# Performance work log

Measured on AMD Instinct MI355X. Metric: run time of the kernel, lower is better.

The kernel has to match this reference:

```python
import jax, jax.numpy as jnp
import numpy as np

E = 1024      # embed_dim
H = 16        # num_heads
D = E // H    # head_dim
SCALING = float(D * 1.0) ** (-0.5)


def setup_inputs() -> dict:
    key = jax.random.key(0)
    ks = jax.random.split(key, 10)
    B, L, S = 4, 2048, 2048
    query = jax.random.normal(ks[0], (B, L, E), dtype=jnp.float32)
    k_in = jax.random.normal(ks[1], (B, S, E), dtype=jnp.float32)
    v_in = jax.random.normal(ks[2], (B, S, E), dtype=jnp.float32)
    attn_bias = jax.random.normal(ks[3], (L, S), dtype=jnp.float32)
    attn_mask = jax.random.normal(ks[4], (L, S), dtype=jnp.float32)
    # in_proj: Linear(E, 3E)  (xavier-uniform-ish scale), out_proj: Linear(E, E)
    lim_in = np.sqrt(6.0 / (E + 3 * E))
    Wqkv = jax.random.uniform(ks[5], (3 * E, E), minval=-lim_in, maxval=lim_in, dtype=jnp.float32)
    bqkv = jnp.zeros((3 * E,), dtype=jnp.float32)
    lim_out = np.sqrt(1.0 / E)
    Wo = jax.random.uniform(ks[6], (E, E), minval=-lim_out, maxval=lim_out, dtype=jnp.float32)
    bo = jnp.zeros((E,), dtype=jnp.float32)
    return {"query": query, "key": k_in, "value": v_in,
            "attn_bias": attn_bias, "attn_mask": attn_mask,
            "Wqkv": Wqkv, "bqkv": bqkv, "Wo": Wo, "bo": bo}


def reference(query, key, value, attn_bias, attn_mask, Wqkv, bqkv, Wo, bo):
    B, L, _ = query.shape
    S = key.shape[1]
    # fused in_proj split into q/k/v slices (q from query, k from key, v from value)
    q = query @ Wqkv[:E].T + bqkv[:E]
    k = key @ Wqkv[E:2 * E].T + bqkv[E:2 * E]
    v = value @ Wqkv[2 * E:].T + bqkv[2 * E:]
    q = q * SCALING
    # [B, L, H, D]
    q = q.reshape(B, L, H, D)
    k = k.reshape(B, S, H, D)
    v = v.reshape(B, S, H, D)
    # scores: [B, H, L, S] with additive float mask and bias (broadcast over B, H)
    scores = jnp.einsum("blhd,bshd->bhls", q, k)
    scores = scores + attn_mask[None, None] + attn_bias[None, None]
    weights = jax.nn.softmax(scores, axis=-1)  # dropout p=0.0 -> identity
    out = jnp.einsum("bhls,bshd->blhd", weights, v).reshape(B, L, E)
    return out @ Wo.T + bo
```

## Files before the change

kernel.cpp:

```cpp
#include <hip/hip_runtime.h>
#include <hip/hip_bf16.h>

#define BB 4
#define LL 2048
#define SS 2048
#define EE 1024
#define HH 16
#define DD 64
#define MM (BB * LL)

typedef unsigned short u16;
typedef u16   u16x4  __attribute__((ext_vector_type(4)));
typedef u16   u16x8  __attribute__((ext_vector_type(8)));
typedef float f32x4  __attribute__((ext_vector_type(4)));
typedef __bf16 bf16x8 __attribute__((ext_vector_type(8)));

__device__ __forceinline__ u16 f2bf(float x) {
    unsigned u = __float_as_uint(x);
    u += 0x7fffu + ((u >> 16) & 1u);
    return (u16)(u >> 16);
}
__device__ __forceinline__ float bf2f(u16 b) {
    return __uint_as_float(((unsigned)b) << 16);
}

__global__ __launch_bounds__(256) void f32_to_bf16_kernel(
    const float* __restrict__ in, u16* __restrict__ out)
{
    size_t idx = ((size_t)blockIdx.x * 256 + threadIdx.x) * 8;
    f32x4 a = *(const f32x4*)(in + idx);
    f32x4 b = *(const f32x4*)(in + idx + 4);
    u16x8 o;
#pragma unroll
    for (int j = 0; j < 4; j++) { o[j] = f2bf(a[j]); o[4 + j] = f2bf(b[j]); }
    *(u16x8*)(out + idx) = o;
}

__global__ __launch_bounds__(256) void combine_bias_kernel(
    const float* __restrict__ bias, const float* __restrict__ mask,
    u16* __restrict__ comb)
{
    int idx = (blockIdx.x * 256 + threadIdx.x) * 8;
    f32x4 a0 = *(const f32x4*)(bias + idx);
    f32x4 a1 = *(const f32x4*)(bias + idx + 4);
    f32x4 m0 = *(const f32x4*)(mask + idx);
    f32x4 m1 = *(const f32x4*)(mask + idx + 4);
    u16x8 o;
#pragma unroll
    for (int j = 0; j < 4; j++) { o[j] = f2bf(a0[j] + m0[j]); o[4 + j] = f2bf(a1[j] + m1[j]); }
    *(u16x8*)(comb + idx) = o;
}

template <int ABF16, int OUTBF16>
__global__ __launch_bounds__(256, 2) void gemm_bt(
    const void* __restrict__ Ap, const u16* __restrict__ Bw,
    const float* __restrict__ bias, void* __restrict__ Cp,
    int M, int N, int K, float scale)
{
    __shared__ __align__(16) u16 As[128 * 72];
    __shared__ __align__(16) u16 Bs[128 * 72];
    const int tid = threadIdx.x;
    const int lane = tid & 63, wave = tid >> 6;
    const int quad = lane >> 4, ln = lane & 15;
    const int wm = (wave & 1) * 64, wn = (wave >> 1) * 64;
    const int m0 = blockIdx.x * 128, n0 = blockIdx.y * 128;

    f32x4 acc[4][4];
#pragma unroll
    for (int mt = 0; mt < 4; mt++)
#pragma unroll
        for (int nt = 0; nt < 4; nt++) acc[mt][nt] = (f32x4){0.f, 0.f, 0.f, 0.f};

    const float* Af = (const float*)Ap;
    const u16*   Ab = (const u16*)Ap;

    f32x4 apf[8];
    u16x8 apb[4];
    u16x8 bpf[4];

    auto load_tiles = [&](int k0) {
        if (ABF16) {
#pragma unroll
            for (int i = 0; i < 4; i++) {
                int chunk = tid + 256 * i, row = chunk >> 3, c = chunk & 7;
                apb[i] = *(const u16x8*)(Ab + (size_t)(m0 + row) * K + k0 + c * 8);
            }
        } else {
#pragma unroll
            for (int i = 0; i < 8; i++) {
                int chunk = tid + 256 * i, row = chunk >> 4, c = chunk & 15;
                apf[i] = *(const f32x4*)(Af + (size_t)(m0 + row) * K + k0 + c * 4);
            }
        }
#pragma unroll
        for (int i = 0; i < 4; i++) {
            int chunk = tid + 256 * i, row = chunk >> 3, c = chunk & 7;
            bpf[i] = *(const u16x8*)(Bw + (size_t)(n0 + row) * K + k0 + c * 8);
        }
    };

    load_tiles(0);

    for (int k0 = 0; k0 < K; k0 += 64) {
        __syncthreads();
        if (ABF16) {
#pragma unroll
            for (int i = 0; i < 4; i++) {
                int chunk = tid + 256 * i, row = chunk >> 3, c = chunk & 7;
                *(u16x8*)(As + row * 72 + c * 8) = apb[i];
            }
        } else {
#pragma unroll
            for (int i = 0; i < 8; i++) {
                int chunk = tid + 256 * i, row = chunk >> 4, c = chunk & 15;
                u16x4 o;
#pragma unroll
                for (int j = 0; j < 4; j++) o[j] = f2bf(apf[i][j]);
                *(u16x4*)(As + row * 72 + c * 4) = o;
            }
        }
#pragma unroll
        for (int i = 0; i < 4; i++) {
            int chunk = tid + 256 * i, row = chunk >> 3, c = chunk & 7;
            *(u16x8*)(Bs + row * 72 + c * 8) = bpf[i];
        }
        __syncthreads();

        if (k0 + 64 < K) load_tiles(k0 + 64);

#pragma unroll
        for (int ks = 0; ks < 2; ks++) {
            bf16x8 af[4], bfg[4];
#pragma unroll
            for (int mt = 0; mt < 4; mt++)
                af[mt] = *(const bf16x8*)(As + (wm + mt * 16 + ln) * 72 + ks * 32 + quad * 8);
#pragma unroll
            for (int nt = 0; nt < 4; nt++)
                bfg[nt] = *(const bf16x8*)(Bs + (wn + nt * 16 + ln) * 72 + ks * 32 + quad * 8);
#pragma unroll
            for (int mt = 0; mt < 4; mt++)
#pragma unroll
                for (int nt = 0; nt < 4; nt++)
                    acc[mt][nt] = __builtin_amdgcn_mfma_f32_16x16x32_bf16(
                        af[mt], bfg[nt], acc[mt][nt], 0, 0, 0);
        }
    }

#pragma unroll
    for (int nt = 0; nt < 4; nt++) {
        int n = n0 + wn + nt * 16 + ln;
        float bn = bias[n];
#pragma unroll
        for (int mt = 0; mt < 4; mt++) {
#pragma unroll
            for (int r = 0; r < 4; r++) {
                int m = m0 + wm + mt * 16 + quad * 4 + r;
                float val = (acc[mt][nt][r] + bn) * scale;
                if (OUTBF16) ((u16*)Cp)[(size_t)m * N + n] = f2bf(val);
                else         ((float*)Cp)[(size_t)m * N + n] = val;
            }
        }
    }
}

__global__ __launch_bounds__(256) void transpose_v_kernel(
    const u16* __restrict__ vb, u16* __restrict__ vt)
{
    __shared__ __align__(16) u16 t[64 * 72];
    const int bh = blockIdx.y, b = bh >> 4, h = bh & 15;
    const int s0 = blockIdx.x * 64;
    const int tid = threadIdx.x;
#pragma unroll
    for (int i = 0; i < 2; i++) {
        int chunk = tid + 256 * i;
        int row = chunk >> 3, c = chunk & 7;
        u16x8 v = *(const u16x8*)(vb + (size_t)(b * SS + s0 + row) * EE + h * 64 + c * 8);
        *(u16x8*)(t + row * 72 + c * 8) = v;
    }
    __syncthreads();
#pragma unroll
    for (int i = 0; i < 2; i++) {
        int chunk = tid + 256 * i;
        int d = chunk >> 3, c = chunk & 7;
        u16x8 o;
#pragma unroll
        for (int j = 0; j < 8; j++) o[j] = t[(c * 8 + j) * 72 + d];
        *(u16x8*)(vt + (size_t)(bh * 64 + d) * SS + s0 + c * 8) = o;
    }
}

__global__ __launch_bounds__(256, 2) void attn_kernel(
    const u16* __restrict__ qb,
    const u16* __restrict__ kb,
    const u16* __restrict__ vt,
    const u16* __restrict__ comb,
    u16* __restrict__ attn)
{
    __shared__ __align__(16) u16 KPs[128 * 136];
    __shared__ __align__(16) u16 Vs[64 * 136];
    const int tid = threadIdx.x, lane = tid & 63, wave = tid >> 6;
    const int quad = lane >> 4, ln = lane & 15;
    const int bh = blockIdx.y, b = bh >> 4, h = bh & 15;
    const int q0 = blockIdx.x * 128;
    const int qloc0 = wave * 32;

    bf16x8 qf[2][2];
#pragma unroll
    for (int qg = 0; qg < 2; qg++)
#pragma unroll
        for (int ks = 0; ks < 2; ks++)
            qf[qg][ks] = *(const bf16x8*)(qb + (size_t)(b * LL + q0 + qloc0 + 16 * qg + ln) * EE
                                          + h * 64 + ks * 32 + quad * 8);

    const u16* cb0 = comb + (size_t)(q0 + qloc0 + ln) * SS + quad * 4;
    const u16* cb1 = cb0 + (size_t)16 * SS;

    f32x4 o[4][2];
#pragma unroll
    for (int mt = 0; mt < 4; mt++) { o[mt][0] = (f32x4){0,0,0,0}; o[mt][1] = (f32x4){0,0,0,0}; }
    float lsum0 = 0.f, lsum1 = 0.f;

    u16x8 kreg[4], vreg[4];
    auto load_kv = [&](int s0) {
#pragma unroll
        for (int i = 0; i < 4; i++) {
            int chunk = tid + 256 * i, row = chunk >> 3, c = chunk & 7;
            kreg[i] = *(const u16x8*)(kb + (size_t)(b * SS + s0 + row) * EE + h * 64 + c * 8);
        }
#pragma unroll
        for (int i = 0; i < 4; i++) {
            int chunk = tid + 256 * i, row = chunk >> 4, c = chunk & 15;
            vreg[i] = *(const u16x8*)(vt + (size_t)(bh * 64 + row) * SS + s0 + c * 8);
        }
    };
    load_kv(0);

    for (int s0 = 0; s0 < SS; s0 += 128) {
        __syncthreads();
#pragma unroll
        for (int i = 0; i < 4; i++) {
            int chunk = tid + 256 * i, row = chunk >> 3, c = chunk & 7;
            *(u16x8*)(KPs + row * 72 + c * 8) = kreg[i];
        }
#pragma unroll
        for (int i = 0; i < 4; i++) {
            int chunk = tid + 256 * i, row = chunk >> 4, c = chunk & 15;
            *(u16x8*)(Vs + row * 136 + c * 8) = vreg[i];
        }
        __syncthreads();

        if (s0 + 128 < SS) load_kv(s0 + 128);

        u16x4 bfr[8][2];
#pragma unroll
        for (int mt = 0; mt < 8; mt++) {
            bfr[mt][0] = *(const u16x4*)(cb0 + s0 + mt * 16);
            bfr[mt][1] = *(const u16x4*)(cb1 + s0 + mt * 16);
        }

        f32x4 st[8][2];
#pragma unroll
        for (int mt = 0; mt < 8; mt++) {
            bf16x8 a0 = *(const bf16x8*)(KPs + (mt * 16 + ln) * 72 + quad * 8);
            bf16x8 a1 = *(const bf16x8*)(KPs + (mt * 16 + ln) * 72 + 32 + quad * 8);
#pragma unroll
            for (int qg = 0; qg < 2; qg++) {
                f32x4 z = (f32x4){0,0,0,0};
                z = __builtin_amdgcn_mfma_f32_16x16x32_bf16(a0, qf[qg][0], z, 0, 0, 0);
                z = __builtin_amdgcn_mfma_f32_16x16x32_bf16(a1, qf[qg][1], z, 0, 0, 0);
                st[mt][qg] = z;
            }
        }

        u16x4 p[8][2];
#pragma unroll
        for (int mt = 0; mt < 8; mt++)
#pragma unroll
            for (int qg = 0; qg < 2; qg++) {
#pragma unroll
                for (int r = 0; r < 4; r++) {
                    float e = __expf(st[mt][qg][r] + bf2f(bfr[mt][qg][r]));
                    if (qg == 0) lsum0 += e; else lsum1 += e;
                    p[mt][qg][r] = f2bf(e);
                }
            }

        __syncthreads();

#pragma unroll
        for (int mt = 0; mt < 8; mt++) {
            *(u16x4*)(KPs + (qloc0 + ln) * 136 + mt * 16 + quad * 4)      = p[mt][0];
            *(u16x4*)(KPs + (qloc0 + 16 + ln) * 136 + mt * 16 + quad * 4) = p[mt][1];
        }

#pragma unroll
        for (int ks = 0; ks < 4; ks++) {
            bf16x8 pf0 = *(const bf16x8*)(KPs + (qloc0 + ln) * 136 + ks * 32 + quad * 8);
            bf16x8 pf1 = *(const bf16x8*)(KPs + (qloc0 + 16 + ln) * 136 + ks * 32 + quad * 8);
#pragma unroll
            for (int mt = 0; mt < 4; mt++) {
                bf16x8 a = *(const bf16x8*)(Vs + (mt * 16 + ln) * 136 + ks * 32 + quad * 8);
                o[mt][0] = __builtin_amdgcn_mfma_f32_16x16x32_bf16(a, pf0, o[mt][0], 0, 0, 0);
                o[mt][1] = __builtin_amdgcn_mfma_f32_16x16x32_bf16(a, pf1, o[mt][1], 0, 0, 0);
            }
        }
    }

    lsum0 += __shfl_xor(lsum0, 16); lsum0 += __shfl_xor(lsum0, 32);
    lsum1 += __shfl_xor(lsum1, 16); lsum1 += __shfl_xor(lsum1, 32);
    float inv0 = 1.f / lsum0, inv1 = 1.f / lsum1;

#pragma unroll
    for (int mt = 0; mt < 4; mt++) {
        u16x4 p0, p1;
#pragma unroll
        for (int r = 0; r < 4; r++) { p0[r] = f2bf(o[mt][0][r] * inv0); p1[r] = f2bf(o[mt][1][r] * inv1); }
        *(u16x4*)(KPs + (qloc0 + ln) * 136 + mt * 16 + quad * 4)      = p0;
        *(u16x4*)(KPs + (qloc0 + 16 + ln) * 136 + mt * 16 + quad * 4) = p1;
    }
#pragma unroll
    for (int i = 0; i < 4; i++) {
        int j = lane + 64 * i;
        int r = j >> 3, c = j & 7;
        u16x8 v = *(const u16x8*)(KPs + (qloc0 + r) * 136 + c * 8);
        *(u16x8*)(attn + (size_t)(b * LL + q0 + qloc0 + r) * EE + h * 64 + c * 8) = v;
    }
}

extern "C" void kernel_launch(void* const* d_in, const int* in_sizes, int n_in,
                              void* d_out, int out_size, void* d_ws, size_t ws_size,
                              hipStream_t stream)
{
    (void)in_sizes; (void)n_in; (void)out_size; (void)ws_size;
    const float* query     = (const float*)d_in[0];
    const float* key       = (const float*)d_in[1];
    const float* value     = (const float*)d_in[2];
    const float* attn_bias = (const float*)d_in[3];
    const float* attn_mask = (const float*)d_in[4];
    const float* Wqkv      = (const float*)d_in[5];
    const float* bqkv      = (const float*)d_in[6];
    const float* Wo        = (const float*)d_in[7];
    const float* bo        = (const float*)d_in[8];
    float* out = (float*)d_out;

    u16* wq_bf = (u16*)d_ws;
    u16* wo_bf = wq_bf + 3 * EE * EE;
    u16* comb  = wo_bf + EE * EE;
    u16* q_bf  = comb + (size_t)LL * SS;
    u16* k_bf  = q_bf + (size_t)MM * EE;
    u16* v_bf  = k_bf + (size_t)MM * EE;
    u16* vtr   = v_bf + (size_t)MM * EE;
    u16* attnb = vtr  + (size_t)MM * EE;

    f32_to_bf16_kernel<<<3 * EE * EE / 2048, 256, 0, stream>>>(Wqkv, wq_bf);
    f32_to_bf16_kernel<<<EE * EE / 2048, 256, 0, stream>>>(Wo, wo_bf);
    combine_bias_kernel<<<(LL * SS) / 2048, 256, 0, stream>>>(attn_bias, attn_mask, comb);

    dim3 gg(MM / 128, EE / 128);
    gemm_bt<0, 1><<<gg, 256, 0, stream>>>(query, wq_bf,               bqkv,          q_bf, MM, EE, EE, 0.125f);
    gemm_bt<0, 1><<<gg, 256, 0, stream>>>(key,   wq_bf + EE * EE,     bqkv + EE,     k_bf, MM, EE, EE, 1.f);
    gemm_bt<0, 1><<<gg, 256, 0, stream>>>(value, wq_bf + 2 * EE * EE, bqkv + 2 * EE, v_bf, MM, EE, EE, 1.f);

    transpose_v_kernel<<<dim3(SS / 64, BB * HH), 256, 0, stream>>>(v_bf, vtr);

    attn_kernel<<<dim3(LL / 128, BB * HH), 256, 0, stream>>>(q_bf, k_bf, vtr, comb, attnb);

    gemm_bt<1, 0><<<gg, 256, 0, stream>>>(attnb, wo_bf, bo, out, MM, EE, EE, 1.f);
}
```

Before: 443.1 us.

## Rework GEMM to direct global-to-LDS loads, fuse V transpose, exp2 softmax

The activations are converted to bf16 up front, and the GEMM now uses global_load_lds with an XOR-swizzled LDS layout instead of register staging. The V projection is computed as W·Xᵀ, writing V already transposed, which removes the transpose kernel. The attention kernel reads K and V fragments straight from global memory instead of staging them in LDS. Softmax folds log2e into the Q scale and the bias so it can use exp2, and packs P by truncation. Workspace buffers are aliased, occupancy hints are raised to 3, and the GEMM drops its register prefetch, so global latency is no longer hidden by the old double-buffer scheme.

```diff
diff --git a/kernel.cpp b/kernel.cpp
--- a/kernel.cpp
+++ b/kernel.cpp
@@ -6,12 +6,15 @@
 #define SS 2048
 #define EE 1024
 #define HH 16
-#define DD 64
 #define MM (BB * LL)
 
+#define LOG2E 1.44269504088896f
+
 typedef unsigned short u16;
+typedef unsigned int   u32;
 typedef u16   u16x4  __attribute__((ext_vector_type(4)));
 typedef u16   u16x8  __attribute__((ext_vector_type(8)));
+typedef u32   u32x2  __attribute__((ext_vector_type(2)));
 typedef float f32x4  __attribute__((ext_vector_type(4)));
 typedef __bf16 bf16x8 __attribute__((ext_vector_type(8)));
 
@@ -23,6 +26,15 @@
 __device__ __forceinline__ float bf2f(u16 b) {
     return __uint_as_float(((unsigned)b) << 16);
 }
+__device__ __forceinline__ u32 pack_trunc(float e0, float e1) {
+    return __builtin_amdgcn_perm(__float_as_uint(e1), __float_as_uint(e0), 0x07060302u);
+}
+__device__ __forceinline__ void glds16(const u16* g, u16* l) {
+    __builtin_amdgcn_global_load_lds(
+        (const __attribute__((address_space(1))) unsigned int*)(size_t)g,
+        (__attribute__((address_space(3))) unsigned int*)(unsigned int)(size_t)l,
+        16, 0, 0);
+}
 
 __global__ __launch_bounds__(256) void f32_to_bf16_kernel(
     const float* __restrict__ in, u16* __restrict__ out)
@@ -40,30 +52,35 @@
     const float* __restrict__ bias, const float* __restrict__ mask,
     u16* __restrict__ comb)
 {
-    int idx = (blockIdx.x * 256 + threadIdx.x) * 8;
+    size_t idx = ((size_t)blockIdx.x * 256 + threadIdx.x) * 8;
     f32x4 a0 = *(const f32x4*)(bias + idx);
     f32x4 a1 = *(const f32x4*)(bias + idx + 4);
     f32x4 m0 = *(const f32x4*)(mask + idx);
     f32x4 m1 = *(const f32x4*)(mask + idx + 4);
     u16x8 o;
 #pragma unroll
-    for (int j = 0; j < 4; j++) { o[j] = f2bf(a0[j] + m0[j]); o[4 + j] = f2bf(a1[j] + m1[j]); }
+    for (int j = 0; j < 4; j++) {
+        o[j]     = f2bf(LOG2E * (a0[j] + m0[j]));
+        o[4 + j] = f2bf(LOG2E * (a1[j] + m1[j]));
+    }
     *(u16x8*)(comb + idx) = o;
 }
 
-template <int ABF16, int OUTBF16>
-__global__ __launch_bounds__(256, 2) void gemm_bt(
-    const void* __restrict__ Ap, const u16* __restrict__ Bw,
+template <int BIASM, int OUTBF16>
+__global__ __launch_bounds__(256, 3) void gemm_bt(
+    const u16* __restrict__ A, const u16* __restrict__ B,
     const float* __restrict__ bias, void* __restrict__ Cp,
     int M, int N, int K, float scale)
 {
-    __shared__ __align__(16) u16 As[128 * 72];
-    __shared__ __align__(16) u16 Bs[128 * 72];
+    __shared__ __align__(16) u16 As[128 * 64];
+    __shared__ __align__(16) u16 Bs[128 * 64];
     const int tid = threadIdx.x;
     const int lane = tid & 63, wave = tid >> 6;
     const int quad = lane >> 4, ln = lane & 15;
     const int wm = (wave & 1) * 64, wn = (wave >> 1) * 64;
     const int m0 = blockIdx.x * 128, n0 = blockIdx.y * 128;
+    const int rl = lane >> 3, cc = lane & 7;
+    const int sc = cc ^ rl;
 
     f32x4 acc[4][4];
 #pragma unroll
@@ -71,72 +88,30 @@
 #pragma unroll
         for (int nt = 0; nt < 4; nt++) acc[mt][nt] = (f32x4){0.f, 0.f, 0.f, 0.f};
 
-    const float* Af = (const float*)Ap;
-    const u16*   Ab = (const u16*)Ap;
-
-    f32x4 apf[8];
-    u16x8 apb[4];
-    u16x8 bpf[4];
-
-    auto load_tiles = [&](int k0) {
-        if (ABF16) {
-#pragma unroll
-            for (int i = 0; i < 4; i++) {
-                int chunk = tid + 256 * i, row = chunk >> 3, c = chunk & 7;
-                apb[i] = *(const u16x8*)(Ab + (size_t)(m0 + row) * K + k0 + c * 8);
-            }
-        } else {
-#pragma unroll
-            for (int i = 0; i < 8; i++) {
-                int chunk = tid + 256 * i, row = chunk >> 4, c = chunk & 15;
-                apf[i] = *(const f32x4*)(Af + (size_t)(m0 + row) * K + k0 + c * 4);
-            }
-        }
+    const int lnx = ln & 7;
+
+    for (int k0 = 0; k0 < K; k0 += 64) {
 #pragma unroll
         for (int i = 0; i < 4; i++) {
-            int chunk = tid + 256 * i, row = chunk >> 3, c = chunk & 7;
-            bpf[i] = *(const u16x8*)(Bw + (size_t)(n0 + row) * K + k0 + c * 8);
-        }
-    };
-
-    load_tiles(0);
-
-    for (int k0 = 0; k0 < K; k0 += 64) {
+            int ch = wave * 4 + i;
+            glds16(A + (size_t)(m0 + ch * 8 + rl) * K + k0 + sc * 8, As + ch * 512);
+            glds16(B + (size_t)(n0 + ch * 8 + rl) * K + k0 + sc * 8, Bs + ch * 512);
+        }
         __syncthreads();
-        if (ABF16) {
-#pragma unroll
-            for (int i = 0; i < 4; i++) {
-                int chunk = tid + 256 * i, row = chunk >> 3, c = chunk & 7;
-                *(u16x8*)(As + row * 72 + c * 8) = apb[i];
-            }
-        } else {
-#pragma unroll
-            for (int i = 0; i < 8; i++) {
-                int chunk = tid + 256 * i, row = chunk >> 4, c = chunk & 15;
-                u16x4 o;
-#pragma unroll
-                for (int j = 0; j < 4; j++) o[j] = f2bf(apf[i][j]);
-                *(u16x4*)(As + row * 72 + c * 4) = o;
-            }
-        }
-#pragma unroll
-        for (int i = 0; i < 4; i++) {
-            int chunk = tid + 256 * i, row = chunk >> 3, c = chunk & 7;
-            *(u16x8*)(Bs + row * 72 + c * 8) = bpf[i];
-        }
-        __syncthreads();
-
-        if (k0 + 64 < K) load_tiles(k0 + 64);
 
 #pragma unroll
         for (int ks = 0; ks < 2; ks++) {
             bf16x8 af[4], bfg[4];
 #pragma unroll
-            for (int mt = 0; mt < 4; mt++)
-                af[mt] = *(const bf16x8*)(As + (wm + mt * 16 + ln) * 72 + ks * 32 + quad * 8);
-#pragma unroll
-            for (int nt = 0; nt < 4; nt++)
-                bfg[nt] = *(const bf16x8*)(Bs + (wn + nt * 16 + ln) * 72 + ks * 32 + quad * 8);
+            for (int mt = 0; mt < 4; mt++) {
+                int row = wm + mt * 16 + ln;
+                af[mt] = *(const bf16x8*)(As + row * 64 + ((ks * 4 + quad) ^ lnx) * 8);
+            }
+#pragma unroll
+            for (int nt = 0; nt < 4; nt++) {
+                int row = wn + nt * 16 + ln;
+                bfg[nt] = *(const bf16x8*)(Bs + row * 64 + ((ks * 4 + quad) ^ lnx) * 8);
+            }
 #pragma unroll
             for (int mt = 0; mt < 4; mt++)
 #pragma unroll
@@ -144,18 +119,21 @@
                     acc[mt][nt] = __builtin_amdgcn_mfma_f32_16x16x32_bf16(
                         af[mt], bfg[nt], acc[mt][nt], 0, 0, 0);
         }
-    }
-
-#pragma unroll
-    for (int nt = 0; nt < 4; nt++) {
-        int n = n0 + wn + nt * 16 + ln;
-        float bn = bias[n];
-#pragma unroll
-        for (int mt = 0; mt < 4; mt++) {
+        __syncthreads();
+    }
+
+#pragma unroll
+    for (int mt = 0; mt < 4; mt++) {
+        f32x4 bm;
+        if (BIASM) bm = *(const f32x4*)(bias + m0 + wm + mt * 16 + quad * 4);
+#pragma unroll
+        for (int nt = 0; nt < 4; nt++) {
+            int n = n0 + wn + nt * 16 + ln;
+            float bn = BIASM ? 0.f : bias[n];
 #pragma unroll
             for (int r = 0; r < 4; r++) {
                 int m = m0 + wm + mt * 16 + quad * 4 + r;
-                float val = (acc[mt][nt][r] + bn) * scale;
+                float val = (acc[mt][nt][r] + (BIASM ? bm[r] : bn)) * scale;
                 if (OUTBF16) ((u16*)Cp)[(size_t)m * N + n] = f2bf(val);
                 else         ((float*)Cp)[(size_t)m * N + n] = val;
             }
@@ -163,41 +141,14 @@
     }
 }
 
-__global__ __launch_bounds__(256) void transpose_v_kernel(
-    const u16* __restrict__ vb, u16* __restrict__ vt)
-{
-    __shared__ __align__(16) u16 t[64 * 72];
-    const int bh = blockIdx.y, b = bh >> 4, h = bh & 15;
-    const int s0 = blockIdx.x * 64;
-    const int tid = threadIdx.x;
-#pragma unroll
-    for (int i = 0; i < 2; i++) {
-        int chunk = tid + 256 * i;
-        int row = chunk >> 3, c = chunk & 7;
-        u16x8 v = *(const u16x8*)(vb + (size_t)(b * SS + s0 + row) * EE + h * 64 + c * 8);
-        *(u16x8*)(t + row * 72 + c * 8) = v;
-    }
-    __syncthreads();
-#pragma unroll
-    for (int i = 0; i < 2; i++) {
-        int chunk = tid + 256 * i;
-        int d = chunk >> 3, c = chunk & 7;
-        u16x8 o;
-#pragma unroll
-        for (int j = 0; j < 8; j++) o[j] = t[(c * 8 + j) * 72 + d];
-        *(u16x8*)(vt + (size_t)(bh * 64 + d) * SS + s0 + c * 8) = o;
-    }
-}
-
-__global__ __launch_bounds__(256, 2) void attn_kernel(
+__global__ __launch_bounds__(256, 3) void attn_kernel(
     const u16* __restrict__ qb,
     const u16* __restrict__ kb,
     const u16* __restrict__ vt,
     const u16* __restrict__ comb,
     u16* __restrict__ attn)
 {
-    __shared__ __align__(16) u16 KPs[128 * 136];
-    __shared__ __align__(16) u16 Vs[64 * 136];
+    __shared__ __align__(16) u16 Ps[128 * 136];
     const int tid = threadIdx.x, lane = tid & 63, wave = tid >> 6;
     const int quad = lane >> 4, ln = lane & 15;
     const int bh = blockIdx.y, b = bh >> 4, h = bh & 15;
@@ -212,6 +163,8 @@
             qf[qg][ks] = *(const bf16x8*)(qb + (size_t)(b * LL + q0 + qloc0 + 16 * qg + ln) * EE
                                           + h * 64 + ks * 32 + quad * 8);
 
+    const u16* kbase = kb + (size_t)b * SS * EE + h * 64;
+    const u16* vbase = vt + (size_t)(h * 64) * MM + b * SS;
     const u16* cb0 = comb + (size_t)(q0 + qloc0 + ln) * SS + quad * 4;
     const u16* cb1 = cb0 + (size_t)16 * SS;
 
@@ -220,88 +173,44 @@
     for (int mt = 0; mt < 4; mt++) { o[mt][0] = (f32x4){0,0,0,0}; o[mt][1] = (f32x4){0,0,0,0}; }
     float lsum0 = 0.f, lsum1 = 0.f;
 
-    u16x8 kreg[4], vreg[4];
-    auto load_kv = [&](int s0) {
-#pragma unroll
-        for (int i = 0; i < 4; i++) {
-            int chunk = tid + 256 * i, row = chunk >> 3, c = chunk & 7;
-            kreg[i] = *(const u16x8*)(kb + (size_t)(b * SS + s0 + row) * EE + h * 64 + c * 8);
-        }
-#pragma unroll
-        for (int i = 0; i < 4; i++) {
-            int chunk = tid + 256 * i, row = chunk >> 4, c = chunk & 15;
-            vreg[i] = *(const u16x8*)(vt + (size_t)(bh * 64 + row) * SS + s0 + c * 8);
-        }
-    };
-    load_kv(0);
+    u16* prow0 = Ps + (qloc0 + ln) * 136;
+    u16* prow1 = Ps + (qloc0 + 16 + ln) * 136;
 
     for (int s0 = 0; s0 < SS; s0 += 128) {
-        __syncthreads();
-#pragma unroll
-        for (int i = 0; i < 4; i++) {
-            int chunk = tid + 256 * i, row = chunk >> 3, c = chunk & 7;
-            *(u16x8*)(KPs + row * 72 + c * 8) = kreg[i];
-        }
-#pragma unroll
-        for (int i = 0; i < 4; i++) {
-            int chunk = tid + 256 * i, row = chunk >> 4, c = chunk & 15;
-            *(u16x8*)(Vs + row * 136 + c * 8) = vreg[i];
-        }
-        __syncthreads();
-
-        if (s0 + 128 < SS) load_kv(s0 + 128);
-
-        u16x4 bfr[8][2];
 #pragma unroll
         for (int mt = 0; mt < 8; mt++) {
-            bfr[mt][0] = *(const u16x4*)(cb0 + s0 + mt * 16);
-            bfr[mt][1] = *(const u16x4*)(cb1 + s0 + mt * 16);
-        }
-
-        f32x4 st[8][2];
-#pragma unroll
-        for (int mt = 0; mt < 8; mt++) {
-            bf16x8 a0 = *(const bf16x8*)(KPs + (mt * 16 + ln) * 72 + quad * 8);
-            bf16x8 a1 = *(const bf16x8*)(KPs + (mt * 16 + ln) * 72 + 32 + quad * 8);
+            const u16* ka = kbase + (size_t)(s0 + mt * 16 + ln) * EE;
+            bf16x8 a0 = *(const bf16x8*)(ka + quad * 8);
+            bf16x8 a1 = *(const bf16x8*)(ka + 32 + quad * 8);
 #pragma unroll
             for (int qg = 0; qg < 2; qg++) {
                 f32x4 z = (f32x4){0,0,0,0};
                 z = __builtin_amdgcn_mfma_f32_16x16x32_bf16(a0, qf[qg][0], z, 0, 0, 0);
                 z = __builtin_amdgcn_mfma_f32_16x16x32_bf16(a1, qf[qg][1], z, 0, 0, 0);
-                st[mt][qg] = z;
-            }
-        }
-
-        u16x4 p[8][2];
-#pragma unroll
-        for (int mt = 0; mt < 8; mt++)
-#pragma unroll
-            for (int qg = 0; qg < 2; qg++) {
-#pragma unroll
-                for (int r = 0; r < 4; r++) {
-                    float e = __expf(st[mt][qg][r] + bf2f(bfr[mt][qg][r]));
-                    if (qg == 0) lsum0 += e; else lsum1 += e;
-                    p[mt][qg][r] = f2bf(e);
-                }
-            }
-
-        __syncthreads();
-
-#pragma unroll
-        for (int mt = 0; mt < 8; mt++) {
-            *(u16x4*)(KPs + (qloc0 + ln) * 136 + mt * 16 + quad * 4)      = p[mt][0];
-            *(u16x4*)(KPs + (qloc0 + 16 + ln) * 136 + mt * 16 + quad * 4) = p[mt][1];
+                u16x4 bv = *(const u16x4*)((qg ? cb1 : cb0) + s0 + mt * 16);
+                float e0 = __builtin_amdgcn_exp2f(z[0] + bf2f(bv[0]));
+                float e1 = __builtin_amdgcn_exp2f(z[1] + bf2f(bv[1]));
+                float e2 = __builtin_amdgcn_exp2f(z[2] + bf2f(bv[2]));
+                float e3 = __builtin_amdgcn_exp2f(z[3] + bf2f(bv[3]));
+                if (qg == 0) lsum0 += (e0 + e1) + (e2 + e3);
+                else         lsum1 += (e0 + e1) + (e2 + e3);
+                u32x2 pk;
+                pk[0] = pack_trunc(e0, e1);
+                pk[1] = pack_trunc(e2, e3);
+                *(u32x2*)((qg ? prow1 : prow0) + mt * 16 + quad * 4) = pk;
+            }
         }
 
 #pragma unroll
         for (int ks = 0; ks < 4; ks++) {
-            bf16x8 pf0 = *(const bf16x8*)(KPs + (qloc0 + ln) * 136 + ks * 32 + quad * 8);
-            bf16x8 pf1 = *(const bf16x8*)(KPs + (qloc0 + 16 + ln) * 136 + ks * 32 + quad * 8);
+            bf16x8 pf0 = *(const bf16x8*)(prow0 + ks * 32 + quad * 8);
+            bf16x8 pf1 = *(const bf16x8*)(prow1 + ks * 32 + quad * 8);
 #pragma unroll
             for (int mt = 0; mt < 4; mt++) {
-                bf16x8 a = *(const bf16x8*)(Vs + (mt * 16 + ln) * 136 + ks * 32 + quad * 8);
-                o[mt][0] = __builtin_amdgcn_mfma_f32_16x16x32_bf16(a, pf0, o[mt][0], 0, 0, 0);
-                o[mt][1] = __builtin_amdgcn_mfma_f32_16x16x32_bf16(a, pf1, o[mt][1], 0, 0, 0);
+                bf16x8 va = *(const bf16x8*)(vbase + (size_t)(mt * 16 + ln) * MM
+                                             + s0 + ks * 32 + quad * 8);
+                o[mt][0] = __builtin_amdgcn_mfma_f32_16x16x32_bf16(va, pf0, o[mt][0], 0, 0, 0);
+                o[mt][1] = __builtin_amdgcn_mfma_f32_16x16x32_bf16(va, pf1, o[mt][1], 0, 0, 0);
             }
         }
     }
@@ -315,14 +224,14 @@
         u16x4 p0, p1;
 #pragma unroll
         for (int r = 0; r < 4; r++) { p0[r] = f2bf(o[mt][0][r] * inv0); p1[r] = f2bf(o[mt][1][r] * inv1); }
-        *(u16x4*)(KPs + (qloc0 + ln) * 136 + mt * 16 + quad * 4)      = p0;
-        *(u16x4*)(KPs + (qloc0 + 16 + ln) * 136 + mt * 16 + quad * 4) = p1;
+        *(u16x4*)(prow0 + mt * 16 + quad * 4) = p0;
+        *(u16x4*)(prow1 + mt * 16 + quad * 4) = p1;
     }
 #pragma unroll
     for (int i = 0; i < 4; i++) {
         int j = lane + 64 * i;
         int r = j >> 3, c = j & 7;
-        u16x8 v = *(const u16x8*)(KPs + (qloc0 + r) * 136 + c * 8);
+        u16x8 v = *(const u16x8*)(Ps + (qloc0 + r) * 136 + c * 8);
         *(u16x8*)(attn + (size_t)(b * LL + q0 + qloc0 + r) * EE + h * 64 + c * 8) = v;
     }
 }
@@ -343,27 +252,34 @@
     const float* bo        = (const float*)d_in[8];
     float* out = (float*)d_out;
 
-    u16* wq_bf = (u16*)d_ws;
-    u16* wo_bf = wq_bf + 3 * EE * EE;
-    u16* comb  = wo_bf + EE * EE;
-    u16* q_bf  = comb + (size_t)LL * SS;
-    u16* k_bf  = q_bf + (size_t)MM * EE;
-    u16* v_bf  = k_bf + (size_t)MM * EE;
-    u16* vtr   = v_bf + (size_t)MM * EE;
-    u16* attnb = vtr  + (size_t)MM * EE;
+    u16* wq_bf  = (u16*)d_ws;
+    u16* wo_bf  = wq_bf + 3 * EE * EE;
+    u16* comb   = wo_bf + EE * EE;
+    u16* qin_bf = comb   + (size_t)LL * SS;
+    u16* kin_bf = qin_bf + (size_t)MM * EE;
+    u16* vin_bf = kin_bf + (size_t)MM * EE;
+    u16* q_bf   = vin_bf + (size_t)MM * EE;
+    u16* vtr    = q_bf   + (size_t)MM * EE;
+    u16* k_bf   = qin_bf;
+    u16* attnb  = kin_bf;
 
     f32_to_bf16_kernel<<<3 * EE * EE / 2048, 256, 0, stream>>>(Wqkv, wq_bf);
     f32_to_bf16_kernel<<<EE * EE / 2048, 256, 0, stream>>>(Wo, wo_bf);
+    f32_to_bf16_kernel<<<(size_t)MM * EE / 2048, 256, 0, stream>>>(query, qin_bf);
+    f32_to_bf16_kernel<<<(size_t)MM * EE / 2048, 256, 0, stream>>>(key, kin_bf);
+    f32_to_bf16_kernel<<<(size_t)MM * EE / 2048, 256, 0, stream>>>(value, vin_bf);
     combine_bias_kernel<<<(LL * SS) / 2048, 256, 0, stream>>>(attn_bias, attn_mask, comb);
 
     dim3 gg(MM / 128, EE / 128);
-    gemm_bt<0, 1><<<gg, 256, 0, stream>>>(query, wq_bf,               bqkv,          q_bf, MM, EE, EE, 0.125f);
-    gemm_bt<0, 1><<<gg, 256, 0, stream>>>(key,   wq_bf + EE * EE,     bqkv + EE,     k_bf, MM, EE, EE, 1.f);
-    gemm_bt<0, 1><<<gg, 256, 0, stream>>>(value, wq_bf + 2 * EE * EE, bqkv + 2 * EE, v_bf, MM, EE, EE, 1.f);
-
-    transpose_v_kernel<<<dim3(SS / 64, BB * HH), 256, 0, stream>>>(v_bf, vtr);
+    gemm_bt<0, 1><<<gg, 256, 0, stream>>>(qin_bf, wq_bf, bqkv, q_bf,
+                                          MM, EE, EE, 0.125f * LOG2E);
+    gemm_bt<0, 1><<<gg, 256, 0, stream>>>(kin_bf, wq_bf + EE * EE, bqkv + EE, k_bf,
+                                          MM, EE, EE, 1.f);
+    dim3 gv(EE / 128, MM / 128);
+    gemm_bt<1, 1><<<gv, 256, 0, stream>>>(wq_bf + 2 * EE * EE, vin_bf, bqkv + 2 * EE, vtr,
+                                          EE, MM, EE, 1.f);
 
     attn_kernel<<<dim3(LL / 128, BB * HH), 256, 0, stream>>>(q_bf, k_bf, vtr, comb, attnb);
 
-    gemm_bt<1, 0><<<gg, 256, 0, stream>>>(attnb, wo_bf, bo, out, MM, EE, EE, 1.f);
-}
+    gemm_bt<0, 0><<<gg, 256, 0, stream>>>(attnb, wo_bf, bo, out, MM, EE, EE, 1.f);
+}
```

Result: slower. 699.0 us (+57.8%).
